# Optimization experiments

Measured on AMD Instinct MI355X. Metric: run time of the kernel, lower is better.

## Reference

```python
import jax, jax.numpy as jnp
import numpy as np

B, S, E, H, ROT, MAXP = 2, 1024, 2048, 16, 64, 2048
HD = E // H
EPS = 1e-12  # torch F.normalize default eps


def _sinusoidal_positions(num_pos, dim):
    # GPT-J create_sinusoidal_positions: concat(sin, cos) along feature dim
    inv_freq = 1.0 / (10000.0 ** (np.arange(0, dim, 2, dtype=np.float32) / dim))
    sinusoid = np.einsum("i,j->ij", np.arange(num_pos, dtype=np.float32), inv_freq)
    return jnp.asarray(np.concatenate([np.sin(sinusoid), np.cos(sinusoid)], axis=-1))


def _rotate_every_two(x):
    x1 = x[..., ::2]
    x2 = x[..., 1::2]
    return jnp.stack((-x2, x1), axis=-1).reshape(x.shape)


def _apply_rotary(t, sin, cos):
    # t: [B,S,H,rot]; sin/cos: [B,S,rot/2] -> repeat_interleave(2) -> [B,S,1,rot]
    sin = jnp.repeat(sin, 2, axis=-1)[:, :, None, :]
    cos = jnp.repeat(cos, 2, axis=-1)[:, :, None, :]
    return t * cos + _rotate_every_two(t) * sin


def setup_inputs() -> dict:
    key = jax.random.key(0)
    ks = jax.random.split(key, 5)
    hidden_states = jax.random.normal(ks[0], (B, S, E), dtype=jnp.float32)
    w_q = jax.random.normal(ks[1], (E, E), dtype=jnp.float32) * 0.02
    w_k = jax.random.normal(ks[2], (E, E), dtype=jnp.float32) * 0.02
    w_v = jax.random.normal(ks[3], (E, E), dtype=jnp.float32) * 0.02
    w_o = jax.random.normal(ks[4], (E, E), dtype=jnp.float32) * 0.02
    norm_const = 0.5 * jnp.ones((1, H, 1, 1), dtype=jnp.float32)
    attention_mask = jnp.zeros((B, 1, 1, S), dtype=jnp.float32)  # 0 = attend (HF additive mask)
    position_ids = jnp.tile(jnp.arange(S, dtype=jnp.int32)[None, :], (B, 1))
    return {"hidden_states": hidden_states, "w_q": w_q, "w_k": w_k, "w_v": w_v,
            "w_o": w_o, "norm_const": norm_const, "attention_mask": attention_mask,
            "position_ids": position_ids}


def reference(hidden_states, w_q, w_k, w_v, w_o, norm_const, attention_mask, position_ids):
    b, s, e = hidden_states.shape
    # projections (nn.Linear, no bias): y = x @ W.T
    q = (hidden_states @ w_q.T).reshape(b, s, H, HD)  # rotary layout [B,S,H,hd]
    k = (hidden_states @ w_k.T).reshape(b, s, H, HD)
    v = (hidden_states @ w_v.T).reshape(b, s, H, HD).transpose(0, 2, 1, 3)  # [B,H,S,hd]

    embed = _sinusoidal_positions(MAXP, ROT)          # [MAXP, ROT]
    sincos = embed[position_ids]                      # [B,S,ROT]
    sin, cos = jnp.split(sincos, 2, axis=-1)          # each [B,S,ROT/2]

    # partial rotary on first ROT dims
    q = jnp.concatenate([_apply_rotary(q[..., :ROT], sin, cos), q[..., ROT:]], axis=-1)
    k = jnp.concatenate([_apply_rotary(k[..., :ROT], sin, cos), k[..., ROT:]], axis=-1)
    q = q.transpose(0, 2, 1, 3)  # [B,H,S,hd]
    k = k.transpose(0, 2, 1, 3)

    causal = jnp.tril(jnp.ones((s, s), dtype=bool))[None, None]   # [1,1,S,S]
    mask0 = (attention_mask == 0)                                  # [B,1,1,S] bool

    # value rescale: per-query count of visible keys ** sigmoid(norm_const), clamped >= 1
    counts = jnp.sum(causal & mask0, axis=-1, keepdims=True).astype(jnp.float32)  # [B,1,S,1]
    denom = jnp.maximum(counts ** jax.nn.sigmoid(norm_const), 1.0)                # [B,H,S,1]
    v = v / denom

    # L2-normalize q/k (torch F.normalize: x / max(||x||, eps))
    q = q / jnp.maximum(jnp.linalg.norm(q, axis=-1, keepdims=True), EPS)
    k = k / jnp.maximum(jnp.linalg.norm(k, axis=-1, keepdims=True), EPS)

    mask_t = jnp.swapaxes(mask0, -1, -2)  # [B,1,S,1]
    q = q * mask_t
    k = k * mask_t
    v = v * mask_t

    attn_weights = jnp.einsum("bhqd,bhkd->bhqk", q, k)     # cosine similarities
    attn_weights = jnp.where(causal, attn_weights, 0.0)
    attn_output = jnp.einsum("bhqk,bhkd->bhqd", attn_weights, v)

    attn_output = attn_output.transpose(0, 2, 1, 3).reshape(b, s, e)
    return attn_output @ w_o.T
```

## Files before the change

### kernel.cpp

```cpp
#include <hip/hip_runtime.h>
#include <math.h>

#define B 2
#define S 1024
#define E 2048
#define H 16
#define HD 128
#define ROT 64
#define EPSN 1e-12f

using half8 = __attribute__((ext_vector_type(8))) _Float16;
using half4 = __attribute__((ext_vector_type(4))) _Float16;
using half2 = __attribute__((ext_vector_type(2))) _Float16;
using f32x4 = __attribute__((ext_vector_type(4))) float;

__device__ __forceinline__ void gl_lds16(const void* g, void* l) {
    __builtin_amdgcn_global_load_lds(
        (const __attribute__((address_space(1))) unsigned int*)g,
        (__attribute__((address_space(3))) unsigned int*)l, 16, 0, 0);
}

#define BARX()  asm volatile("s_barrier" ::: "memory")
#define LGKM0() asm volatile("s_waitcnt lgkmcnt(0)" ::: "memory")
#define VMW(n)  asm volatile("s_waitcnt vmcnt(" #n ")" ::: "memory")

__device__ __forceinline__ int ctIdx(int row, int col) {
    return row * 256 + (col & 3) + ((((col >> 2) ^ ((row >> 3) & 15)) & 63) << 2);
}

__global__ __launch_bounds__(256) void f2h5(const float* __restrict__ x0,
                                            const float* __restrict__ x1,
                                            const float* __restrict__ x2,
                                            const float* __restrict__ x3,
                                            const float* __restrict__ x4,
                                            _Float16* __restrict__ y0,
                                            _Float16* __restrict__ y1,
                                            _Float16* __restrict__ y2,
                                            _Float16* __restrict__ y3,
                                            _Float16* __restrict__ y4) {
    const float* xs[5] = {x0, x1, x2, x3, x4};
    _Float16*    ys[5] = {y0, y1, y2, y3, y4};
    const int t = blockIdx.y;
    const int i = blockIdx.x * 256 + threadIdx.x;
    float4 v = ((const float4*)xs[t])[i];
    half4 h;
    h[0] = (_Float16)v.x; h[1] = (_Float16)v.y;
    h[2] = (_Float16)v.z; h[3] = (_Float16)v.w;
    ((half4*)ys[t])[i] = h;
}

__global__ __launch_bounds__(1024) void countprep(const float* __restrict__ am,
                                                  float* __restrict__ cnt) {
    __shared__ float sc[1024];
    const int b = blockIdx.x, t = threadIdx.x;
    sc[t] = (am[b * S + t] == 0.f) ? 1.f : 0.f;
    __syncthreads();
    for (int off = 1; off < 1024; off <<= 1) {
        float u = (t >= off) ? sc[t - off] : 0.f;
        __syncthreads();
        sc[t] += u;
        __syncthreads();
    }
    cnt[b * S + t] = sc[t];
}

__global__ __launch_bounds__(512, 2) void gemm_qkv256(
        const _Float16* __restrict__ hs,
        const _Float16* __restrict__ wq,
        const _Float16* __restrict__ wk,
        const _Float16* __restrict__ wv,
        _Float16* __restrict__ qo,
        _Float16* __restrict__ ko,
        _Float16* __restrict__ kto,
        _Float16* __restrict__ vto,
        const float* __restrict__ am,
        const int*  __restrict__ pos,
        const float* __restrict__ nc,
        const float* __restrict__ cnt) {
    __shared__ uint4 L[8][1024];
    __shared__ float sclA[256], sclB[256];

    const int lid = (int)blockIdx.x;
    const int swz = (lid & 7) * 24 + (lid >> 3);
    const int z   = swz >> 6;
    const int gm  = (swz & 63) >> 3;
    const int gn  = swz & 7;
    const _Float16* Wp = (z == 0) ? wq : (z == 1) ? wk : wv;
    const int mBase = gm << 8;
    const int nBase = gn << 8;

    const int tid   = (int)threadIdx.x;
    const int lane  = tid & 63;
    const int w     = tid >> 6;
    const int l15   = lane & 15;
    const int lq    = lane >> 4;
    const int wm4   = (w >> 2) << 2;
    const int wn2   = (w & 3) << 1;
    const int wbase = tid & 448;

    const int bb  = mBase >> 10;
    const int sB0 = mBase & (S - 1);
    const int h0  = gn * 2;

    if (tid < 256) {
        const int sgx = sB0 + tid;
        float valid = (am[bb * S + sgx] == 0.f) ? 1.f : 0.f;
        if (z == 2) {
            float c  = cnt[bb * S + sgx];
            float g0 = 1.f / (1.f + expf(-nc[h0]));
            float g1 = 1.f / (1.f + expf(-nc[h0 + 1]));
            sclA[tid] = valid / fmaxf(powf(c, g0), 1.f);
            sclB[tid] = valid / fmaxf(powf(c, g1), 1.f);
        } else {
            sclA[tid] = valid;
        }
    }

    f32x4 acc[2][2][4][2];
#pragma unroll
    for (int X = 0; X < 2; ++X)
#pragma unroll
        for (int Y = 0; Y < 2; ++Y)
#pragma unroll
            for (int mt = 0; mt < 4; ++mt)
#pragma unroll
                for (int nt = 0; nt < 2; ++nt)
                    acc[X][Y][mt][nt] = (f32x4){0.f, 0.f, 0.f, 0.f};

    half8 af[4][2], wf[2][2];

    auto stage = [&](int slot, const _Float16* src, int rowBase, int hf, int kt) {
#pragma unroll
        for (int j = 0; j < 2; ++j) {
            const int c  = (j << 9) + tid;
            const int rb = c >> 7;
            const int q  = (c >> 4) & 7;
            const int r  = c & 15;
            gl_lds16(&src[(size_t)(rowBase + hf * 128 + rb * 16 + r) * E +
                          kt * 64 + q * 8],
                     &L[slot][(j << 9) + wbase]);
        }
    };
    auto ldsA = [&](int db, int X) {
#pragma unroll
        for (int mt = 0; mt < 4; ++mt)
#pragma unroll
            for (int ks = 0; ks < 2; ++ks)
                af[mt][ks] = *(const half8*)&L[db * 2 + X]
                    [(wm4 + mt) * 128 + (ks * 4 + lq) * 16 + l15];
    };
    auto ldsB = [&](int db, int Y) {
#pragma unroll
        for (int nt = 0; nt < 2; ++nt)
#pragma unroll
            for (int ks = 0; ks < 2; ++ks)
                wf[nt][ks] = *(const half8*)&L[4 + db * 2 + Y]
                    [(wn2 + nt) * 128 + (ks * 4 + lq) * 16 + l15];
    };
    auto mma = [&](int X, int Y) {
        __builtin_amdgcn_s_setprio(1);
#pragma unroll
        for (int mt = 0; mt < 4; ++mt)
#pragma unroll
            for (int nt = 0; nt < 2; ++nt)
#pragma unroll
                for (int ks = 0; ks < 2; ++ks)
                    acc[X][Y][mt][nt] = __builtin_amdgcn_mfma_f32_16x16x32_f16(
                        af[mt][ks], wf[nt][ks], acc[X][Y][mt][nt], 0, 0, 0);
        __builtin_amdgcn_s_setprio(0);
    };

    stage(0, hs, mBase, 0, 0);
    stage(4, Wp, nBase, 0, 0);
    stage(1, hs, mBase, 1, 0);
    stage(5, Wp, nBase, 1, 0);
    stage(2, hs, mBase, 0, 1);
    stage(7, Wp, nBase, 1, 1);
    stage(3, hs, mBase, 1, 1);
    VMW(6);
    BARX();

    for (int j = 0; j < 16; ++j) {
        const int tB  = 2 * j + 1;
        const int tN0 = 2 * j + 2;
        const int tN1 = 2 * j + 3;
        const bool more = (j < 15);

        ldsA(0, 0); ldsB(0, 0);
        stage(6, Wp, nBase, 0, tB);
        BARX(); LGKM0();
        mma(0, 0);
        BARX();

        ldsB(0, 1);
        if (more) stage(0, hs, mBase, 0, tN0);
        BARX(); LGKM0();
        mma(0, 1);
        BARX();

        ldsA(0, 1);
        if (more) stage(5, Wp, nBase, 1, tN0);
        BARX(); LGKM0();
        mma(1, 1);
        BARX();

        ldsB(0, 0);
        if (more) { stage(1, hs, mBase, 1, tN0); VMW(4); }
        else      { VMW(0); }
        BARX(); LGKM0();
        mma(1, 0);
        BARX();

        ldsA(1, 0); ldsB(1, 0);
        if (more) stage(4, Wp, nBase, 0, tN0);
        BARX(); LGKM0();
        mma(0, 0);
        BARX();

        ldsB(1, 1);
        if (more) stage(2, hs, mBase, 0, tN1);
        BARX(); LGKM0();
        mma(0, 1);
        BARX();

        ldsA(1, 1);
        if (more) stage(7, Wp, nBase, 1, tN1);
        BARX(); LGKM0();
        mma(1, 1);
        BARX();

        ldsB(1, 0);
        if (more) stage(3, hs, mBase, 1, tN1);
        VMW(4);
        BARX(); LGKM0();
        mma(1, 0);
        BARX();
    }

    VMW(0);
    BARX();
    _Float16* CtH = (_Float16*)&L[0][0];
#pragma unroll
    for (int X = 0; X < 2; ++X)
#pragma unroll
        for (int Y = 0; Y < 2; ++Y)
#pragma unroll
            for (int mt = 0; mt < 4; ++mt)
#pragma unroll
                for (int nt = 0; nt < 2; ++nt)
#pragma unroll
                    for (int r = 0; r < 4; ++r) {
                        int row = X * 128 + (w >> 2) * 64 + mt * 16 + lq * 4 + r;
                        int col = Y * 128 + (w & 3) * 32 + nt * 16 + l15;
                        float v = acc[X][Y][mt][nt][r];
                        if (z == 2) v *= (Y ? sclB[row] : sclA[row]);
                        CtH[ctIdx(row, col)] = (_Float16)v;
                    }
    __syncthreads();

    if (z < 2) {
        _Float16* rowOut = (z == 0) ? qo : ko;
        const int hh = lane >> 5;
        const int il = lane & 31;
        for (int rr = 0; rr < 32; ++rr) {
            int row = w * 32 + rr;
            int sg  = sB0 + row;
            float p = (float)pos[bb * S + sg];
            half4 x = *(const half4*)&CtH[ctIdx(row, hh * 128 + il * 4)];
            float v0 = x[0], v1 = x[1], v2 = x[2], v3 = x[3];
            if (il < 16) {
                float a0 = p * expf(-0.28782313662425574f * (float)(2 * il));
                float a1 = p * expf(-0.28782313662425574f * (float)(2 * il + 1));
                float s0, c0, s1, c1;
                sincosf(a0, &s0, &c0);
                sincosf(a1, &s1, &c1);
                float t0 = v0 * c0 - v1 * s0, t1 = v1 * c0 + v0 * s0;
                float t2 = v2 * c1 - v3 * s1, t3 = v3 * c1 + v2 * s1;
                v0 = t0; v1 = t1; v2 = t2; v3 = t3;
            }
            float ss = v0 * v0 + v1 * v1 + v2 * v2 + v3 * v3;
            ss += __shfl_xor(ss, 1);  ss += __shfl_xor(ss, 2);
            ss += __shfl_xor(ss, 4);  ss += __shfl_xor(ss, 8);
            ss += __shfl_xor(ss, 16);
            float scl = sclA[row] / fmaxf(sqrtf(ss), EPSN);
            half4 y;
            y[0] = (_Float16)(v0 * scl); y[1] = (_Float16)(v1 * scl);
            y[2] = (_Float16)(v2 * scl); y[3] = (_Float16)(v3 * scl);
            *(half4*)&rowOut[(((size_t)bb * H + h0 + hh) * S + sg) * HD +
                             il * 4] = y;
            if (z == 1)
                *(half4*)&CtH[ctIdx(row, hh * 128 + il * 4)] = y;
        }
    }
    if (z >= 1) {
        if (z == 1) __syncthreads();
        _Float16* To = (z == 1) ? kto : vto;
#pragma unroll
        for (int i = 0; i < 16; ++i) {
            int cch = tid + i * 512;
            int dr  = cch >> 5;
            int sc  = cch & 31;
            half8 hv;
#pragma unroll
            for (int jj = 0; jj < 8; ++jj)
                hv[jj] = CtH[ctIdx(sc * 8 + jj, dr)];
            *(half8*)&To[(((size_t)bb * H + h0 + (dr >> 7)) * HD + (dr & 127)) * S +
                         sB0 + sc * 8] = hv;
        }
    }
}

__global__ __launch_bounds__(256) void gemm_out(const _Float16* __restrict__ A,
                                                const _Float16* __restrict__ Wp,
                                                float* __restrict__ C) {
    __shared__ uint4 As_l[2][512];
    __shared__ uint4 Ws_l[2][512];
    const int lid = (int)blockIdx.x;
    const int swz = (lid & 7) * 32 + (lid >> 3);
    const int gm  = swz >> 4;
    const int gn  = swz & 15;
    const int tid  = threadIdx.x;
    const int lane = tid & 63;
    const int w    = tid >> 6;
    const int wm   = (w >> 1) * 64;
    const int wn   = (w & 1) * 64;
    const int l15  = lane & 15;
    const int lq   = lane >> 4;
    const int r16  = lane & 15;
    const int kq4  = lane >> 4;
    const int mBase = gm * 128;
    const int nBase = gn * 128;

    f32x4 acc[4][4];
#pragma unroll
    for (int mt = 0; mt < 4; ++mt)
#pragma unroll
        for (int nt = 0; nt < 4; ++nt)
            acc[mt][nt] = (f32x4){0.f, 0.f, 0.f, 0.f};

    auto stage = [&](int bf, int k0) {
#pragma unroll
        for (int i = 0; i < 2; ++i) {
            int rb = w * 2 + i;
            gl_lds16(&A[(size_t)(mBase + rb * 16 + r16) * E + k0 + kq4 * 8],
                     &As_l[bf][rb * 64]);
            gl_lds16(&Wp[(size_t)(nBase + rb * 16 + r16) * E + k0 + kq4 * 8],
                     &Ws_l[bf][rb * 64]);
        }
    };

    stage(0, 0);
    const int nIter = E / 32;
    for (int it = 0; it < nIter; ++it) {
        __syncthreads();
        if (it + 1 < nIter) stage((it + 1) & 1, (it + 1) * 32);

        const int cur = it & 1;
        half8 af[4], wfr[4];
#pragma unroll
        for (int t = 0; t < 4; ++t) {
            int rbA = (wm >> 4) + t;
            int rbW = (wn >> 4) + t;
            af[t]  = *(const half8*)&As_l[cur][rbA * 64 + lq * 16 + l15];
            wfr[t] = *(const half8*)&Ws_l[cur][rbW * 64 + lq * 16 + l15];
        }
#pragma unroll
        for (int mt = 0; mt < 4; ++mt)
#pragma unroll
            for (int nt = 0; nt < 4; ++nt)
                acc[mt][nt] = __builtin_amdgcn_mfma_f32_16x16x32_f16(
                    af[mt], wfr[nt], acc[mt][nt], 0, 0, 0);
    }

#pragma unroll
    for (int mt = 0; mt < 4; ++mt)
#pragma unroll
        for (int nt = 0; nt < 4; ++nt)
#pragma unroll
            for (int r = 0; r < 4; ++r) {
                int row = mBase + wm + mt * 16 + lq * 4 + r;
                int col = nBase + wn + nt * 16 + l15;
                C[(size_t)row * E + col] = acc[mt][nt][r];
            }
}

__global__ __launch_bounds__(256) void kvouter(const _Float16* __restrict__ kt,
                                               const _Float16* __restrict__ vt,
                                               _Float16* __restrict__ ut) {
    __shared__ __align__(16) _Float16 SB[2 * 128 * 72];
    _Float16 (*Kt_s)[72] = (_Float16(*)[72])SB;
    _Float16 (*Vt_s)[72] = (_Float16(*)[72])(SB + 128 * 72);
    const int c  = blockIdx.x;
    const int bh = blockIdx.y;
    const int tid = threadIdx.x;
    const int lane = tid & 63, w = tid >> 6;
    const int l15 = lane & 15, lq = lane >> 4;
    const size_t ds_b = (size_t)bh * HD * S + (size_t)c * 64;

    uint4 pk[4], pv[4];
#pragma unroll
    for (int j = 0; j < 4; ++j) {
        int f = tid + j * 256;
        int d = f >> 3, c8 = f & 7;
        pk[j] = *(const uint4*)&kt[ds_b + (size_t)d * S + c8 * 8];
        pv[j] = *(const uint4*)&vt[ds_b + (size_t)d * S + c8 * 8];
    }
#pragma unroll
    for (int j = 0; j < 4; ++j) {
        int f = tid + j * 256;
        int d = f >> 3, c8 = f & 7;
        *(uint4*)&Kt_s[d][c8 * 8] = pk[j];
        *(uint4*)&Vt_s[d][c8 * 8] = pv[j];
    }
    __syncthreads();

    f32x4 acc[2][8];
#pragma unroll
    for (int mt = 0; mt < 2; ++mt)
#pragma unroll
        for (int nt = 0; nt < 8; ++nt)
            acc[mt][nt] = (f32x4){0.f, 0.f, 0.f, 0.f};

#pragma unroll
    for (int ks = 0; ks < 2; ++ks) {
        half8 af[2], wf[8];
#pragma unroll
        for (int mt = 0; mt < 2; ++mt)
            af[mt] = *(const half8*)&Kt_s[(w * 2 + mt) * 16 + l15][ks * 32 + lq * 8];
#pragma unroll
        for (int nt = 0; nt < 8; ++nt)
            wf[nt] = *(const half8*)&Vt_s[nt * 16 + l15][ks * 32 + lq * 8];
#pragma unroll
        for (int mt = 0; mt < 2; ++mt)
#pragma unroll
            for (int nt = 0; nt < 8; ++nt)
                acc[mt][nt] = __builtin_amdgcn_mfma_f32_16x16x32_f16(
                    af[mt], wf[nt], acc[mt][nt], 0, 0, 0);
    }
    __syncthreads();

    _Float16* Mb = SB;
#pragma unroll
    for (int mt = 0; mt < 2; ++mt)
#pragma unroll
        for (int nt = 0; nt < 8; ++nt)
#pragma unroll
            for (int r = 0; r < 4; ++r) {
                int dk = (w * 2 + mt) * 16 + lq * 4 + r;
                int flat = nt * 2048 + (dk >> 5) * 512 +
                           (l15 + ((dk >> 3) & 3) * 16) * 8 + (dk & 7);
                Mb[flat] = (_Float16)acc[mt][nt][r];
            }
    __syncthreads();

    const size_t ub = ((size_t)bh * 16 + c) << 14;
#pragma unroll
    for (int j = 0; j < 8; ++j) {
        int f = tid + j * 256;
        *(uint4*)&ut[ub + (size_t)f * 8] = *(const uint4*)&Mb[f * 8];
    }
}

__global__ __launch_bounds__(256) void prefix16(_Float16* __restrict__ u) {
    const int sl = blockIdx.x & 7;
    const int bh = blockIdx.x >> 3;
    const size_t base = (size_t)bh * 16 * 16384 + sl * 2048 + threadIdx.x * 8;
    float acc[8] = {0.f, 0.f, 0.f, 0.f, 0.f, 0.f, 0.f, 0.f};
    half8 nxt = *(const half8*)&u[base];
#pragma unroll
    for (int c = 0; c < 16; ++c) {
        half8 cur = nxt;
        if (c < 15) nxt = *(const half8*)&u[base + (size_t)(c + 1) * 16384];
        half8 outv;
#pragma unroll
        for (int i = 0; i < 8; ++i) outv[i] = (_Float16)acc[i];
        *(half8*)&u[base + (size_t)c * 16384] = outv;
#pragma unroll
        for (int i = 0; i < 8; ++i) acc[i] += (float)cur[i];
    }
}

__global__ __launch_bounds__(256) void attn_local(const _Float16* __restrict__ qh,
                                                  const _Float16* __restrict__ kh,
                                                  const _Float16* __restrict__ vt,
                                                  const _Float16* __restrict__ mt,
                                                  _Float16* __restrict__ o) {
    __shared__ _Float16 Ks[64][136];
    __shared__ _Float16 Vs[HD][72];
    __shared__ _Float16 Ps[64][72];
    __shared__ uint4 Ms[2048];

    const int qt = blockIdx.x;
    const int bh = blockIdx.y;
    const int b = bh >> 4, h = bh & 15;
    const int tid = threadIdx.x;
    const int lane = tid & 63;
    const int w = tid >> 6;
    const int l15 = lane & 15;
    const int lq = lane >> 4;
    const int qBase = qt * 64;
    const size_t sd_base = (size_t)bh * S * HD;

    half8 qf[4];
#pragma unroll
    for (int ks = 0; ks < 4; ++ks)
        qf[ks] = *(const half8*)&qh[sd_base + (size_t)(qBase + w * 16 + l15) * HD +
                                    ks * 32 + lq * 8];

    const _Float16* mtc = mt + (((size_t)bh * 16 + qt) << 14);
#pragma unroll
    for (int rr = 0; rr < 8; ++rr)
        gl_lds16(&mtc[(size_t)((rr * 4 + w) * 64 + lane) * 8],
                 &Ms[(rr * 4 + w) * 64]);

    uint4 pk[4], pv[4];
#pragma unroll
    for (int j = 0; j < 4; ++j) {
        int f = tid + j * 256;
        int rK = f >> 4, c8K = f & 15;
        int rV = f >> 3, c8V = f & 7;
        pk[j] = *(const uint4*)&kh[sd_base + (size_t)(qBase + rK) * HD + c8K * 8];
        pv[j] = *(const uint4*)&vt[sd_base + (size_t)rV * S + qBase + c8V * 8];
    }
#pragma unroll
    for (int j = 0; j < 4; ++j) {
        int f = tid + j * 256;
        int rK = f >> 4, c8K = f & 15;
        int rV = f >> 3, c8V = f & 7;
        *(uint4*)&Ks[rK][c8K * 8] = pk[j];
        *(uint4*)&Vs[rV][c8V * 8] = pv[j];
    }
    __syncthreads();

    f32x4 sacc[4];
#pragma unroll
    for (int nt = 0; nt < 4; ++nt)
        sacc[nt] = (f32x4){0.f, 0.f, 0.f, 0.f};
#pragma unroll
    for (int nt = 0; nt < 4; ++nt)
#pragma unroll
        for (int ks = 0; ks < 4; ++ks) {
            half8 kf = *(const half8*)&Ks[nt * 16 + l15][ks * 32 + lq * 8];
            sacc[nt] = __builtin_amdgcn_mfma_f32_16x16x32_f16(qf[ks], kf,
                                                              sacc[nt], 0, 0, 0);
        }

#pragma unroll
    for (int nt = 0; nt < 4; ++nt)
#pragma unroll
        for (int r = 0; r < 4; ++r) {
            int ql = w * 16 + lq * 4 + r;
            int kl = nt * 16 + l15;
            float sv = (kl <= ql) ? sacc[nt][r] : 0.f;
            Ps[ql][kl] = (_Float16)sv;
        }

    f32x4 oacc[8];
#pragma unroll
    for (int dt = 0; dt < 8; ++dt)
        oacc[dt] = (f32x4){0.f, 0.f, 0.f, 0.f};
#pragma unroll
    for (int dt = 0; dt < 8; ++dt)
#pragma unroll
        for (int km = 0; km < 4; ++km) {
            half8 mf = *(const half8*)&Ms[(dt * 4 + km) * 64 + lane];
            oacc[dt] = __builtin_amdgcn_mfma_f32_16x16x32_f16(qf[km], mf,
                                                              oacc[dt], 0, 0, 0);
        }
    __syncthreads();

    half8 pf[2];
    pf[0] = *(const half8*)&Ps[w * 16 + l15][lq * 8];
    pf[1] = *(const half8*)&Ps[w * 16 + l15][32 + lq * 8];
#pragma unroll
    for (int dt = 0; dt < 8; ++dt)
#pragma unroll
        for (int ks = 0; ks < 2; ++ks) {
            half8 vf = *(const half8*)&Vs[dt * 16 + l15][ks * 32 + lq * 8];
            oacc[dt] = __builtin_amdgcn_mfma_f32_16x16x32_f16(pf[ks], vf,
                                                              oacc[dt], 0, 0, 0);
        }

#pragma unroll
    for (int dt = 0; dt < 8; ++dt)
#pragma unroll
        for (int r = 0; r < 4; ++r)
            Ks[w * 16 + lq * 4 + r][dt * 16 + l15] = (_Float16)oacc[dt][r];
    __syncthreads();
#pragma unroll
    for (int j = 0; j < 4; ++j) {
        int f = tid + j * 256;
        int ql = f >> 4, c8 = f & 15;
        *(uint4*)&o[(size_t)(b * S + qBase + ql) * E + h * HD + c8 * 8] =
            *(const uint4*)&Ks[ql][c8 * 8];
    }
}

extern "C" void kernel_launch(void* const* d_in, const int* in_sizes, int n_in,
                              void* d_out, int out_size, void* d_ws, size_t ws_size,
                              hipStream_t stream) {
    (void)in_sizes; (void)n_in; (void)out_size; (void)ws_size;
    const float* hs = (const float*)d_in[0];
    const float* wq = (const float*)d_in[1];
    const float* wk = (const float*)d_in[2];
    const float* wv = (const float*)d_in[3];
    const float* wo = (const float*)d_in[4];
    const float* nc = (const float*)d_in[5];
    const float* am = (const float*)d_in[6];
    const int*  pos = (const int*)d_in[7];
    float* out = (float*)d_out;

    const size_t act = (size_t)B * S * E;
    _Float16* hsb = (_Float16*)d_ws;
    _Float16* wqb = hsb + act;
    _Float16* wkb = wqb + act;
    _Float16* wvb = wkb + act;
    _Float16* wob = wvb + act;
    _Float16* qhh = wob + act;
    _Float16* khh = qhh + act;
    _Float16* ktt = khh + act;
    _Float16* vtt = ktt + act;
    _Float16* abb = vtt + act;
    _Float16* utm = wqb;
    float*    cnt = (float*)abb;

    f2h5<<<dim3((int)(act / 4 / 256), 5), 256, 0, stream>>>(
        hs, wq, wk, wv, wo, hsb, wqb, wkb, wvb, wob);

    countprep<<<B, 1024, 0, stream>>>(am, cnt);

    gemm_qkv256<<<192, 512, 0, stream>>>(hsb, wqb, wkb, wvb,
                                         qhh, khh, ktt, vtt, am, pos, nc, cnt);

    kvouter<<<dim3(16, B * H), 256, 0, stream>>>(ktt, vtt, utm);
    prefix16<<<B * H * 8, 256, 0, stream>>>(utm);
    attn_local<<<dim3(16, B * H), 256, 0, stream>>>(qhh, khh, vtt, utm, abb);

    gemm_out<<<256, 256, 0, stream>>>(abb, wob, out);
}
```

Before: 325.0 us.

## Precompute rotary sin/cos table and restructure q/k normalize epilogue per thread-row

```diff
diff --git a/kernel.cpp b/kernel.cpp
--- a/kernel.cpp
+++ b/kernel.cpp
@@ -25,7 +25,8 @@
 #define VMW(n)  asm volatile("s_waitcnt vmcnt(" #n ")" ::: "memory")
 
 __device__ __forceinline__ int ctIdx(int row, int col) {
-    return row * 256 + (col & 3) + ((((col >> 2) ^ ((row >> 3) & 15)) & 63) << 2);
+    int f = (row & 15) ^ ((row >> 3) & 15);
+    return row * 256 + (col & 3) + (((col >> 2) ^ f) << 2);
 }
 
 __global__ __launch_bounds__(256) void f2h5(const float* __restrict__ x0,
@@ -50,7 +51,9 @@
 }
 
 __global__ __launch_bounds__(1024) void countprep(const float* __restrict__ am,
-                                                  float* __restrict__ cnt) {
+                                                  const int* __restrict__ pos,
+                                                  float* __restrict__ cnt,
+                                                  float* __restrict__ tab) {
     __shared__ float sc[1024];
     const int b = blockIdx.x, t = threadIdx.x;
     sc[t] = (am[b * S + t] == 0.f) ? 1.f : 0.f;
@@ -62,6 +65,17 @@
         __syncthreads();
     }
     cnt[b * S + t] = sc[t];
+
+    const float p = (float)pos[b * S + t];
+    float* tp = &tab[((size_t)b * S + t) * 64];
+#pragma unroll
+    for (int j = 0; j < 32; ++j) {
+        float ang = p * expf(-0.28782313662425574f * (float)j);
+        float s_, c_;
+        sincosf(ang, &s_, &c_);
+        tp[j * 2]     = c_;
+        tp[j * 2 + 1] = s_;
+    }
 }
 
 __global__ __launch_bounds__(512, 2) void gemm_qkv256(
@@ -74,9 +88,9 @@
         _Float16* __restrict__ kto,
         _Float16* __restrict__ vto,
         const float* __restrict__ am,
-        const int*  __restrict__ pos,
         const float* __restrict__ nc,
-        const float* __restrict__ cnt) {
+        const float* __restrict__ cnt,
+        const float* __restrict__ tab) {
     __shared__ uint4 L[8][1024];
     __shared__ float sclA[256], sclB[256];
 
@@ -259,37 +273,44 @@
     __syncthreads();
 
     if (z < 2) {
-        _Float16* rowOut = (z == 0) ? qo : ko;
-        const int hh = lane >> 5;
-        const int il = lane & 31;
-        for (int rr = 0; rr < 32; ++rr) {
-            int row = w * 32 + rr;
-            int sg  = sB0 + row;
-            float p = (float)pos[bb * S + sg];
-            half4 x = *(const half4*)&CtH[ctIdx(row, hh * 128 + il * 4)];
+        const int row = tid >> 1;
+        const int hh  = tid & 1;
+        const int sg  = sB0 + row;
+        const float* tb = &tab[((size_t)bb * S + sg) * 64];
+
+        half4 gv[32];
+        float ss = 0.f;
+#pragma unroll
+        for (int k = 0; k < 32; ++k) {
+            half4 x = *(const half4*)&CtH[ctIdx(row, hh * 128 + k * 4)];
             float v0 = x[0], v1 = x[1], v2 = x[2], v3 = x[3];
-            if (il < 16) {
-                float a0 = p * expf(-0.28782313662425574f * (float)(2 * il));
-                float a1 = p * expf(-0.28782313662425574f * (float)(2 * il + 1));
-                float s0, c0, s1, c1;
-                sincosf(a0, &s0, &c0);
-                sincosf(a1, &s1, &c1);
-                float t0 = v0 * c0 - v1 * s0, t1 = v1 * c0 + v0 * s0;
-                float t2 = v2 * c1 - v3 * s1, t3 = v3 * c1 + v2 * s1;
+            if (k < 16) {
+                float4 t4 = *(const float4*)&tb[k * 4];
+                float t0 = v0 * t4.x - v1 * t4.y;
+                float t1 = v1 * t4.x + v0 * t4.y;
+                float t2 = v2 * t4.z - v3 * t4.w;
+                float t3 = v3 * t4.z + v2 * t4.w;
                 v0 = t0; v1 = t1; v2 = t2; v3 = t3;
             }
-            float ss = v0 * v0 + v1 * v1 + v2 * v2 + v3 * v3;
-            ss += __shfl_xor(ss, 1);  ss += __shfl_xor(ss, 2);
-            ss += __shfl_xor(ss, 4);  ss += __shfl_xor(ss, 8);
-            ss += __shfl_xor(ss, 16);
-            float scl = sclA[row] / fmaxf(sqrtf(ss), EPSN);
+            ss += v0 * v0 + v1 * v1 + v2 * v2 + v3 * v3;
             half4 y;
-            y[0] = (_Float16)(v0 * scl); y[1] = (_Float16)(v1 * scl);
-            y[2] = (_Float16)(v2 * scl); y[3] = (_Float16)(v3 * scl);
-            *(half4*)&rowOut[(((size_t)bb * H + h0 + hh) * S + sg) * HD +
-                             il * 4] = y;
+            y[0] = (_Float16)v0; y[1] = (_Float16)v1;
+            y[2] = (_Float16)v2; y[3] = (_Float16)v3;
+            gv[k] = y;
+        }
+        float scl = sclA[row] / fmaxf(sqrtf(ss), EPSN);
+        _Float16* rowOut = (z == 0) ? qo : ko;
+        _Float16* gp = &rowOut[(((size_t)bb * H + h0 + hh) * S + sg) * HD];
+#pragma unroll
+        for (int k = 0; k < 32; ++k) {
+            half4 y;
+            y[0] = (_Float16)((float)gv[k][0] * scl);
+            y[1] = (_Float16)((float)gv[k][1] * scl);
+            y[2] = (_Float16)((float)gv[k][2] * scl);
+            y[3] = (_Float16)((float)gv[k][3] * scl);
+            *(half4*)&gp[k * 4] = y;
             if (z == 1)
-                *(half4*)&CtH[ctIdx(row, hh * 128 + il * 4)] = y;
+                *(half4*)&CtH[ctIdx(row, hh * 128 + k * 4)] = y;
         }
     }
     if (z >= 1) {
@@ -623,14 +644,15 @@
     _Float16* abb = vtt + act;
     _Float16* utm = wqb;
     float*    cnt = (float*)abb;
+    float*    tab = cnt + B * S;
 
     f2h5<<<dim3((int)(act / 4 / 256), 5), 256, 0, stream>>>(
         hs, wq, wk, wv, wo, hsb, wqb, wkb, wvb, wob);
 
-    countprep<<<B, 1024, 0, stream>>>(am, cnt);
+    countprep<<<B, 1024, 0, stream>>>(am, pos, cnt, tab);
 
     gemm_qkv256<<<192, 512, 0, stream>>>(hsb, wqb, wkb, wvb,
-                                         qhh, khh, ktt, vtt, am, pos, nc, cnt);
+                                         qhh, khh, ktt, vtt, am, nc, cnt, tab);
 
     kvouter<<<dim3(16, B * H), 256, 0, stream>>>(ktt, vtt, utm);
     prefix16<<<B * H * 8, 256, 0, stream>>>(utm);
```

Result: no change. 324.5 us (-0.2%).
